# Kernel tuning notes

Measured on AMD Instinct MI355X. Metric: run time of the kernel, lower is better.

## Reference

```python
import jax, jax.numpy as jnp
import numpy as np

B, S, D, H, HD = 2, 4096, 768, 12, 64
W = 256           # one-sided window (attention_window=512)
C = S // W        # number of query chunks
NEG = -1e9


def _heads(x):
    # [B,S,D] -> [B,H,S,HD]
    return x.reshape(B, S, H, HD).transpose(0, 2, 1, 3)


def setup_inputs() -> dict:
    key = jax.random.key(0)
    ks = jax.random.split(key, 9)
    sc = 0.02
    w = lambda i: jax.random.normal(ks[i], (D, D), jnp.float32) * sc
    return {
        "hidden_states": jax.random.normal(ks[0], (B, S, D), jnp.float32),
        "Wq": w(1), "Wk": w(2), "Wv": w(3),
        "Wqg": w(4), "Wkg": w(5), "Wvg": w(6),
        "Wo": w(7),
        "attention_mask": jnp.ones((B, S), jnp.int32),
    }


def reference(hidden_states, Wq, Wk, Wv, Wqg, Wkg, Wvg, Wo, attention_mask):
    x = hidden_states
    scale = 1.0 / float(np.sqrt(HD))
    q = _heads(x @ Wq) * scale           # [B,H,S,HD]
    k = _heads(x @ Wk)
    v = _heads(x @ Wv)

    # ---- banded sliding-window attention (chunked, no [S,S] matrix) ----
    idx = jnp.arange(C)[:, None] * W + jnp.arange(3 * W)[None, :]   # [C,3W] into padded seq
    key_pos = idx - W                                               # absolute key position
    kp = jnp.pad(k, ((0, 0), (0, 0), (W, W), (0, 0)))
    vp = jnp.pad(v, ((0, 0), (0, 0), (W, W), (0, 0)))
    kc = kp[:, :, idx]                   # [B,H,C,3W,HD]
    vc = vp[:, :, idx]
    qc = q.reshape(B, H, C, W, HD)
    band = jnp.einsum('bhcqd,bhckd->bhcqk', qc, kc)  # [B,H,C,W,3W]

    qi = jnp.arange(W)[:, None]
    kj = jnp.arange(3 * W)[None, :]
    diag_ok = (kj >= qi) & (kj <= qi + 2 * W)              # |i-j| <= W
    valid = (key_pos >= 0) & (key_pos < S) & (key_pos != 0)  # in-range, dedupe global key 0
    mask = diag_ok[None, :, :] & valid[:, None, :]          # [C,W,3W]
    band = jnp.where(mask[None, None], band, NEG)

    # padding mask on keys
    m = jnp.where(attention_mask > 0, 0.0, NEG).astype(jnp.float32)  # [B,S]
    mp = jnp.pad(m, ((0, 0), (W, W)), constant_values=NEG)
    band = band + mp[:, idx][:, None, :, None, :]
    band = band.reshape(B, H, S, 3 * W)

    # every local query also attends to the global (CLS, pos 0) key
    gsc = jnp.einsum('bhsd,bhgd->bhsg', q, k[:, :, 0:1])   # [B,H,S,1]
    gsc = gsc + m[:, 0][:, None, None, None]

    scores = jnp.concatenate([gsc, band], axis=-1)          # [B,H,S,1+3W]
    probs = jax.nn.softmax(scores, axis=-1)
    pg = probs[..., :1]                                     # global-key prob
    pb = probs[..., 1:].reshape(B, H, C, W, 3 * W)
    out = jnp.einsum('bhcqk,bhckd->bhcqd', pb, vc).reshape(B, H, S, HD)
    out = out + pg * v[:, :, 0:1]

    # ---- global query (CLS) full attention with dedicated projections ----
    qg = _heads(x @ Wqg)[:, :, 0:1] * scale                 # [B,H,1,HD]
    kg = _heads(x @ Wkg)
    vg = _heads(x @ Wvg)
    gs = jnp.einsum('bhgd,bhsd->bhgs', qg, kg) + m[:, None, None, :]
    og = jnp.einsum('bhgs,bhsd->bhgd', jax.nn.softmax(gs, axis=-1), vg)
    out = out.at[:, :, 0:1].set(og)

    out = out.transpose(0, 2, 1, 3).reshape(B, S, D) @ Wo
    return out
```

## Files before the change

kernel.cpp:

```cpp
#include <hip/hip_runtime.h>

#define S_LEN 4096
#define NH 12
#define HDIM 64
#define DMODEL 768
#define NEGF -1.0e9f
#define TOK0_SPLITS 16

typedef __attribute__((ext_vector_type(8))) short bf16x8;
typedef __attribute__((ext_vector_type(4))) float f32x4;

__device__ __forceinline__ short f2b(float f) {
  union { float f; unsigned u; } v; v.f = f;
  unsigned r = v.u + 0x7fffu + ((v.u >> 16) & 1u);
  return (short)(r >> 16);
}
__device__ __forceinline__ float b2f(short s) {
  union { unsigned u; float f; } v; v.u = ((unsigned)(unsigned short)s) << 16;
  return v.f;
}

__global__ __launch_bounds__(256) void k_pre(const float* __restrict__ x,
                                             const float* __restrict__ Wq,
                                             const float* __restrict__ Wk,
                                             const float* __restrict__ Wv,
                                             const float* __restrict__ Wkg,
                                             const float* __restrict__ Wvg,
                                             const float* __restrict__ Wo,
                                             const float* __restrict__ Wqg,
                                             const int* __restrict__ amask,
                                             short* __restrict__ xb,
                                             short* __restrict__ W5t,
                                             short* __restrict__ Wot,
                                             float* __restrict__ qg,
                                             float* __restrict__ mvb) {
  __shared__ float smem[1056];
  int bid = blockIdx.x, tid = threadIdx.x;
  if (bid < 6144) {
    int i = bid * 256 + tid;
    float4 v = ((const float4*)x)[i];
    ((short4*)xb)[i] = make_short4(f2b(v.x), f2b(v.y), f2b(v.z), f2b(v.w));
  } else if (bid < 9600) {
    int zb = bid - 6144;
    int z = zb / 576, rem = zb - z * 576;
    int by = rem / 24, bx = rem - by * 24;
    const float* src; float scale = 1.f; short* dst;
    switch (z) {
      case 0: src = Wq;  scale = 0.125f * 1.44269504f; dst = W5t; break;
      case 1: src = Wk;  dst = W5t + 589824; break;
      case 2: src = Wv;  dst = W5t + 2 * 589824; break;
      case 3: src = Wkg; dst = W5t + 3 * 589824; break;
      case 4: src = Wvg; dst = W5t + 4 * 589824; break;
      default: src = Wo; dst = Wot; break;
    }
    int tx = tid & 31, ty = tid >> 5;
    int kb = by * 32, nb = bx * 32;
    for (int i = 0; i < 4; i++) smem[(ty + 8 * i) * 33 + tx] = src[(kb + ty + 8 * i) * 768 + nb + tx];
    __syncthreads();
    for (int i = 0; i < 4; i++)
      dst[(nb + ty + 8 * i) * 768 + kb + tx] = f2b(smem[tx * 33 + ty + 8 * i] * scale);
  } else if (bid < 9632) {
    int zb = bid - 9600;
    int b = zb >> 4, s = (zb & 15) * 256 + tid;
    mvb[b * S_LEN + s] = (s != 0 && amask[b * S_LEN + s] > 0) ? 0.f : NEGF;
  } else {
    int zb = bid - 9632;
    int h = zb % 12, b = zb / 12;
    int out = tid & 63, slice = tid >> 6;
    float* xr = smem;
    float* ps = smem + 768;
    for (int i = tid; i < 768; i += 256) xr[i] = x[(long)b * S_LEN * 768 + i];
    __syncthreads();
    float a = 0.f;
    int n = h * 64 + out;
#pragma unroll 8
    for (int k = slice * 192; k < slice * 192 + 192; k++) a += xr[k] * Wqg[k * 768 + n];
    ps[slice * 64 + out] = a;
    __syncthreads();
    if (tid < 64)
      qg[b * 768 + h * 64 + tid] = (ps[tid] + ps[64 + tid] + ps[128 + tid] + ps[192 + tid]) * 0.125f;
  }
}

__global__ __launch_bounds__(256) void k_gemm(const short* __restrict__ A,
                                              const short* __restrict__ Bt, int K, int mode,
                                              short* __restrict__ qkv, float* __restrict__ outf) {
  __shared__ short Al[2][128 * 32];
  __shared__ short Bl[2][128 * 32];
  int bid = blockIdx.x;
  int xcd = bid & 7, ii = bid >> 3;
  int bm = xcd * 8 + (ii & 7), bn = ii >> 3;
  int tid = threadIdx.x;
  int bm0 = bm * 128, bn0 = bn * 128;
  int w = tid >> 6, lane = tid & 63, g = lane >> 4, r16 = lane & 15;
  int wr = (w >> 1) * 64, wc = (w & 1) * 64;
  f32x4 zero4 = {0.f, 0.f, 0.f, 0.f};
  f32x4 acc[4][4];
  for (int m = 0; m < 4; m++) for (int n = 0; n < 4; n++) acc[m][n] = zero4;
  int srow = w * 32 + (lane >> 2);
  int scol = (lane & 3) * 8;
#define G_STAGE(BUF, KT)                                                              \
  do {                                                                                \
    for (int i = 0; i < 2; i++) {                                                     \
      const short* ga = &A[(long)(bm0 + srow + i * 16) * K + (KT) + scol];            \
      const short* gb = &Bt[(long)(bn0 + srow + i * 16) * K + (KT) + scol];           \
      __builtin_amdgcn_global_load_lds(                                               \
          (const __attribute__((address_space(1))) void*)ga,                          \
          (__attribute__((address_space(3))) void*)&Al[BUF][(w * 32 + i * 16) * 32],  \
          16, 0, 0);                                                                  \
      __builtin_amdgcn_global_load_lds(                                               \
          (const __attribute__((address_space(1))) void*)gb,                          \
          (__attribute__((address_space(3))) void*)&Bl[BUF][(w * 32 + i * 16) * 32],  \
          16, 0, 0);                                                                  \
    }                                                                                 \
  } while (0)
  int nt = K >> 5;
  G_STAGE(0, 0);
  __syncthreads();
  int cur = 0;
  for (int t = 0; t < nt; t++) {
    if (t + 1 < nt) G_STAGE(cur ^ 1, (t + 1) * 32);
    bf16x8 af[4], bfv[4];
    for (int m = 0; m < 4; m++) af[m] = *(const bf16x8*)&Al[cur][(wr + m * 16 + r16) * 32 + g * 8];
    for (int n = 0; n < 4; n++) bfv[n] = *(const bf16x8*)&Bl[cur][(wc + n * 16 + r16) * 32 + g * 8];
    for (int m = 0; m < 4; m++)
      for (int n = 0; n < 4; n++)
        acc[m][n] = __builtin_amdgcn_mfma_f32_16x16x32_bf16(af[m], bfv[n], acc[m][n], 0, 0, 0);
    __syncthreads();
    cur ^= 1;
  }
#undef G_STAGE
  for (int m = 0; m < 4; m++)
    for (int n = 0; n < 4; n++)
      for (int reg = 0; reg < 4; reg++) {
        int row = bm0 + wr + m * 16 + g * 4 + reg;
        int col = bn0 + wc + n * 16 + r16;
        float val = acc[m][n][reg];
        if (mode == 0) {
          int proj = col / 768;
          int rem = col - proj * 768;
          int hh = rem >> 6, d = rem & 63;
          int bb = row >> 12, s = row & 4095;
          qkv[(long)proj * 6291456 + ((((long)bb * NH + hh) * S_LEN + s) << 6) + d] = f2b(val);
        } else {
          outf[(long)row * 768 + col] = val;
        }
      }
}

__global__ __launch_bounds__(256) void k_vt(const short* __restrict__ V, short* __restrict__ Vt) {
  __shared__ short buf[64][72];
  int st = blockIdx.x, bh = blockIdx.y;
  int tid = threadIdx.x;
  long base = (long)bh * S_LEN * HDIM;
  int s0 = st * 64;
  int r = tid >> 2, c = (tid & 3) * 16;
  *(int4*)&buf[r][c]     = *(const int4*)&V[base + (long)(s0 + r) * HDIM + c];
  *(int4*)&buf[r][c + 8] = *(const int4*)&V[base + (long)(s0 + r) * HDIM + c + 8];
  __syncthreads();
  int d = tid >> 2, sc = (tid & 3) * 16;
  short tmp[16];
#pragma unroll
  for (int j = 0; j < 16; j++) tmp[j] = buf[sc + j][d];
  long ob = base + (long)d * S_LEN + s0 + sc;
  *(int4*)&Vt[ob]     = *(const int4*)&tmp[0];
  *(int4*)&Vt[ob + 8] = *(const int4*)&tmp[8];
}

#define KVPAD 36
#define PSTRIDE 68

__device__ __forceinline__ void band_chunk(
    int ks0, int qrow0, int g, int r16,
    const bf16x8 (&qf)[2][2], const bf16x8 (&kf)[4][2], const bf16x8 (&vf)[4][2],
    const float (&mv)[4],
    float (&mstate)[2][4], float (&lstate)[2][4], f32x4 (&acc)[2][4],
    short* Plds) {
  int dlo = ks0 - qrow0;
  bool fullok = (dlo >= -224) && (dlo <= 192);
  for (int m = 0; m < 2; m++) {
    f32x4 s[4];
    f32x4 zero4 = {0.f, 0.f, 0.f, 0.f};
    for (int n = 0; n < 4; n++) {
      f32x4 z = __builtin_amdgcn_mfma_f32_16x16x32_bf16(qf[m][0], kf[n][0], zero4, 0, 0, 0);
      s[n] = __builtin_amdgcn_mfma_f32_16x16x32_bf16(qf[m][1], kf[n][1], z, 0, 0, 0);
    }
    float p[4][4], rmax[4];
    for (int reg = 0; reg < 4; reg++) rmax[reg] = NEGF;
    if (fullok) {
      for (int n = 0; n < 4; n++)
        for (int reg = 0; reg < 4; reg++) {
          float val = s[n][reg] + mv[n];
          p[n][reg] = val;
          rmax[reg] = fmaxf(rmax[reg], val);
        }
    } else {
      int qbase = qrow0 + m * 16 + g * 4;
      for (int n = 0; n < 4; n++) {
        int kpos = ks0 + n * 16 + r16;
        for (int reg = 0; reg < 4; reg++) {
          int qpos = qbase + reg;
          bool ok = (kpos >= qpos - 256) && (kpos <= qpos + 256);
          float val = ok ? (s[n][reg] + mv[n]) : NEGF;
          p[n][reg] = val;
          rmax[reg] = fmaxf(rmax[reg], val);
        }
      }
    }
    for (int reg = 0; reg < 4; reg++) {
      float r = rmax[reg];
      r = fmaxf(r, __shfl_xor(r, 1));
      r = fmaxf(r, __shfl_xor(r, 2));
      r = fmaxf(r, __shfl_xor(r, 4));
      r = fmaxf(r, __shfl_xor(r, 8));
      rmax[reg] = r;
    }
    bool over = false;
    for (int reg = 0; reg < 4; reg++) over = over || (rmax[reg] > mstate[m][reg] + 8.f);
    if (__any((int)over)) {
      float scal[4];
      for (int reg = 0; reg < 4; reg++) {
        float mn = fmaxf(mstate[m][reg], rmax[reg]);
        scal[reg] = __builtin_amdgcn_exp2f(mstate[m][reg] - mn);
        mstate[m][reg] = mn;
      }
      float rs[4] = {0.f, 0.f, 0.f, 0.f};
      for (int n = 0; n < 4; n++)
        for (int reg = 0; reg < 4; reg++) {
          float e = __builtin_amdgcn_exp2f(p[n][reg] - mstate[m][reg]);
          p[n][reg] = e;
          rs[reg] += e;
        }
      for (int reg = 0; reg < 4; reg++) {
        float r = rs[reg];
        r += __shfl_xor(r, 1);
        r += __shfl_xor(r, 2);
        r += __shfl_xor(r, 4);
        r += __shfl_xor(r, 8);
        lstate[m][reg] = lstate[m][reg] * scal[reg] + r;
      }
      for (int n = 0; n < 4; n++)
        for (int reg = 0; reg < 4; reg++) acc[m][n][reg] *= scal[reg];
    } else {
      float rs[4] = {0.f, 0.f, 0.f, 0.f};
      for (int n = 0; n < 4; n++)
        for (int reg = 0; reg < 4; reg++) {
          float e = __builtin_amdgcn_exp2f(p[n][reg] - mstate[m][reg]);
          p[n][reg] = e;
          rs[reg] += e;
        }
      for (int reg = 0; reg < 4; reg++) {
        float r = rs[reg];
        r += __shfl_xor(r, 1);
        r += __shfl_xor(r, 2);
        r += __shfl_xor(r, 4);
        r += __shfl_xor(r, 8);
        lstate[m][reg] += r;
      }
    }
    for (int n = 0; n < 4; n++)
      for (int reg = 0; reg < 4; reg++)
        Plds[(g * 4 + reg) * PSTRIDE + n * 16 + r16] = f2b(p[n][reg]);
    bf16x8 pa[2];
    for (int ks = 0; ks < 2; ks++)
      pa[ks] = *(const bf16x8*)&Plds[r16 * PSTRIDE + ks * 32 + g * 8];
    for (int n = 0; n < 4; n++)
      for (int ks = 0; ks < 2; ks++)
        acc[m][n] = __builtin_amdgcn_mfma_f32_16x16x32_bf16(pa[ks], vf[n][ks], acc[m][n], 0, 0, 0);
  }
}

__global__ __launch_bounds__(256, 2) void k_band(const short* __restrict__ Qb,
                                                 const short* __restrict__ Kb,
                                                 const short* __restrict__ Vb,
                                                 const short* __restrict__ Vtb,
                                                 const int* __restrict__ amask,
                                                 const float* __restrict__ mvb,
                                                 short* __restrict__ oattn) {
  int qtb = blockIdx.x, h = blockIdx.y, b = blockIdx.z;
  int tid = threadIdx.x, w = tid >> 6, lane = tid & 63, g = lane >> 4, r16 = lane & 15;
  long bhof = ((long)(b * NH + h)) * S_LEN * HDIM;
  __shared__ short Klds[2][2][64][KVPAD];
  __shared__ short Vlds[2][2][64][KVPAD];
  __shared__ short Plds[4][16 * PSTRIDE];
  int qb0 = qtb * 128;
  int qrow0 = qb0 + w * 32;

  bf16x8 qf[2][2];
  for (int m = 0; m < 2; m++)
    for (int ks = 0; ks < 2; ks++)
      qf[m][ks] = *(const bf16x8*)&Qb[bhof + (long)(qrow0 + m * 16 + r16) * HDIM + ks * 32 + g * 8];

  float mstate[2][4], lstate[2][4];
  f32x4 acc[2][4];
  {
    bf16x8 k0f[2];
    for (int ks = 0; ks < 2; ks++) k0f[ks] = *(const bf16x8*)&Kb[bhof + ks * 32 + g * 8];
    float part[2];
    for (int m = 0; m < 2; m++) {
      float p = 0.f;
      for (int ks = 0; ks < 2; ks++)
        for (int j = 0; j < 8; j++) p += b2f(qf[m][ks][j]) * b2f(k0f[ks][j]);
      p += __shfl_xor(p, 16);
      p += __shfl_xor(p, 32);
      part[m] = p;
    }
    float mask0 = (amask[b * S_LEN] > 0) ? 0.f : NEGF;
    float v0v[4];
    for (int n = 0; n < 4; n++) v0v[n] = b2f(Vb[bhof + n * 16 + r16]);
    for (int m = 0; m < 2; m++)
      for (int reg = 0; reg < 4; reg++) {
        mstate[m][reg] = __shfl(part[m], g * 4 + reg) + mask0;
        lstate[m][reg] = 1.f;
        for (int n = 0; n < 4; n++) acc[m][n][reg] = v0v[n];
      }
  }

  int c0 = (qb0 - 256) >> 6; if (c0 < 0) c0 = 0;
  int c1 = (qb0 + 127 + 256) >> 6; if (c1 > 63) c1 = 63;
  int wlo = (qrow0 - 256) >> 6;
  int whi = (qrow0 + 31 + 256) >> 6;

  int ss = tid >> 2, qq = tid & 3;
  int ksh = qq >> 1, qcol = (qq & 1) * 16;
  int4 rk0, rk1, rv0, rv1;
#define STAGE_LOAD(CI)                                                              \
  do {                                                                              \
    int _k = (CI) * 64;                                                             \
    const int4* gk = (const int4*)&Kb[bhof + (long)(_k + ss) * HDIM + qq * 16];     \
    rk0 = gk[0]; rk1 = gk[1];                                                       \
    const int4* gv = (const int4*)&Vtb[bhof + (long)ss * S_LEN + _k + qq * 16];     \
    rv0 = gv[0]; rv1 = gv[1];                                                       \
  } while (0)
#define STAGE_WRITE(BUF)                                                            \
  do {                                                                              \
    short* kd = &Klds[BUF][ksh][ss][qcol];                                          \
    *(int4*)kd = rk0; *(int4*)(kd + 8) = rk1;                                       \
    short* vd = &Vlds[BUF][ksh][ss][qcol];                                          \
    *(int4*)vd = rv0; *(int4*)(vd + 8) = rv1;                                       \
  } while (0)

  STAGE_LOAD(c0);
  STAGE_WRITE(0);
  __syncthreads();

  for (int ci = c0; ci <= c1; ci++) {
    int buf = (ci - c0) & 1;
    bool havenext = (ci + 1 <= c1);
    if (havenext) STAGE_LOAD(ci + 1);
    if (ci >= wlo && ci <= whi) {
      int ks0 = ci * 64;
      bf16x8 kf[4][2], vf[4][2];
      for (int n = 0; n < 4; n++)
        for (int ks = 0; ks < 2; ks++) {
          kf[n][ks] = *(const bf16x8*)&Klds[buf][ks][n * 16 + r16][g * 8];
          vf[n][ks] = *(const bf16x8*)&Vlds[buf][ks][n * 16 + r16][g * 8];
        }
      float mv[4];
      for (int n = 0; n < 4; n++) mv[n] = mvb[b * S_LEN + ks0 + n * 16 + r16];
      band_chunk(ks0, qrow0, g, r16, qf, kf, vf, mv, mstate, lstate, acc, &Plds[w][0]);
    }
    if (havenext) STAGE_WRITE(buf ^ 1);
    __syncthreads();
  }
#undef STAGE_LOAD
#undef STAGE_WRITE

  for (int m = 0; m < 2; m++)
    for (int n = 0; n < 4; n++)
      for (int reg = 0; reg < 4; reg++) {
        int token = qrow0 + m * 16 + g * 4 + reg;
        int col = h * 64 + n * 16 + r16;
        oattn[((long)b * S_LEN + token) * 768 + col] = f2b(acc[m][n][reg] / lstate[m][reg]);
      }
}

__global__ __launch_bounds__(256) void k_tok0_part(const float* __restrict__ qg,
                                                   const short* __restrict__ Kg,
                                                   const short* __restrict__ Vg,
                                                   const int* __restrict__ amask,
                                                   float* __restrict__ part) {
  int split = blockIdx.x, bhid = blockIdx.y;
  int b = bhid / NH, h = bhid % NH;
  long base = (long)bhid * S_LEN * HDIM;
  int tid = threadIdx.x, lane = tid & 63, w = tid >> 6;
  int s = split * 256 + tid;
  __shared__ float qgl[64];
  __shared__ float p_sh[256];
  __shared__ float red[4];
  __shared__ float psum[4][64];
  if (tid < 64) qgl[tid] = qg[b * 768 + h * 64 + tid];
  __syncthreads();
  float dot = 0.f;
  {
    const int4* kr = (const int4*)&Kg[base + (long)s * HDIM];
#pragma unroll
    for (int u = 0; u < 8; u++) {
      int4 pk = kr[u];
      const short* sp = (const short*)&pk;
      for (int j = 0; j < 8; j++) dot += qgl[u * 8 + j] * b2f(sp[j]);
    }
    dot += (amask[b * S_LEN + s] > 0) ? 0.f : NEGF;
  }
  float mx = dot;
  for (int o = 32; o; o >>= 1) mx = fmaxf(mx, __shfl_xor(mx, o));
  if (lane == 0) red[w] = mx;
  __syncthreads();
  mx = fmaxf(fmaxf(red[0], red[1]), fmaxf(red[2], red[3]));
  float e = __expf(dot - mx);
  p_sh[tid] = e;
  float sum = e;
  for (int o = 32; o; o >>= 1) sum += __shfl_xor(sum, o);
  __syncthreads();
  if (lane == 0) red[w] = sum;
  __syncthreads();
  sum = red[0] + red[1] + red[2] + red[3];
  int d = tid & 63, grp = tid >> 6;
  float a = 0.f;
  long vb = base + (long)(split * 256 + grp * 64) * HDIM + d;
#pragma unroll 8
  for (int j = 0; j < 64; j++) a += p_sh[grp * 64 + j] * b2f(Vg[vb + (long)j * HDIM]);
  psum[grp][d] = a;
  __syncthreads();
  float* dst = &part[((long)bhid * TOK0_SPLITS + split) * 66];
  if (tid == 0) { dst[0] = mx; dst[1] = sum; }
  if (tid < 64) dst[2 + tid] = psum[0][tid] + psum[1][tid] + psum[2][tid] + psum[3][tid];
}

__global__ void k_tok0_comb(const float* __restrict__ part, short* __restrict__ oattn) {
  int bhid = blockIdx.x, d = threadIdx.x;
  int b = bhid / NH, h = bhid % NH;
  const float* p0 = &part[(long)bhid * TOK0_SPLITS * 66];
  float M = NEGF;
  for (int i = 0; i < TOK0_SPLITS; i++) M = fmaxf(M, p0[i * 66]);
  float L = 0.f, a = 0.f;
  for (int i = 0; i < TOK0_SPLITS; i++) {
    float sc = __expf(p0[i * 66] - M);
    L += sc * p0[i * 66 + 1];
    a += sc * p0[i * 66 + 2 + d];
  }
  oattn[((long)b * S_LEN) * 768 + h * 64 + d] = f2b(a / L);
}

extern "C" void kernel_launch(void* const* d_in, const int* in_sizes, int n_in,
                              void* d_out, int out_size, void* d_ws, size_t ws_size,
                              hipStream_t stream) {
  (void)in_sizes; (void)n_in; (void)out_size; (void)ws_size;
  const float* x   = (const float*)d_in[0];
  const float* Wq  = (const float*)d_in[1];
  const float* Wk  = (const float*)d_in[2];
  const float* Wv  = (const float*)d_in[3];
  const float* Wqg = (const float*)d_in[4];
  const float* Wkg = (const float*)d_in[5];
  const float* Wvg = (const float*)d_in[6];
  const float* Wo  = (const float*)d_in[7];
  const int* amask = (const int*)d_in[8];
  char* ws = (char*)d_ws;
  short* xb    = (short*)(ws);
  short* Vt    = (short*)(ws);
  short* W5t   = (short*)(ws + 12582912);
  short* Wot   = (short*)(ws + 18481152);
  short* qkv   = (short*)(ws + 19660800);
  short* oattn = (short*)(ws + 82575360);
  float* qgbuf = (float*)(ws + 95158272);
  float* partb = (float*)(ws + 95164416);
  float* mvb   = (float*)(ws + 95265792);
  float* outf  = (float*)d_out;

  k_pre<<<9656, 256, 0, stream>>>(x, Wq, Wk, Wv, Wkg, Wvg, Wo, Wqg, amask,
                                  xb, W5t, Wot, qgbuf, mvb);
  k_gemm<<<1920, 256, 0, stream>>>(xb, W5t, 768, 0, qkv, nullptr);
  const short* Qb = qkv;
  const short* Kb = qkv + 6291456;
  const short* Vb = qkv + 2 * 6291456;
  const short* Kg = qkv + 3 * 6291456;
  const short* Vg = qkv + 4 * 6291456;
  k_vt<<<dim3(64, 24), 256, 0, stream>>>(Vb, Vt);
  k_band<<<dim3(32, 12, 2), 256, 0, stream>>>(Qb, Kb, Vb, Vt, amask, mvb, oattn);
  k_tok0_part<<<dim3(TOK0_SPLITS, 24), 256, 0, stream>>>(qgbuf, Kg, Vg, amask, partb);
  k_tok0_comb<<<24, 64, 0, stream>>>(partb, oattn);
  k_gemm<<<384, 256, 0, stream>>>(oattn, Wot, 768, 1, nullptr, outf);
}
```

Baseline: 215.2 us.

## Merge band attention and global-token partial kernels into one launch

```diff
diff --git a/kernel.cpp b/kernel.cpp
--- a/kernel.cpp
+++ b/kernel.cpp
@@ -270,161 +270,163 @@
   }
 }
 
-__global__ __launch_bounds__(256, 2) void k_band(const short* __restrict__ Qb,
+__global__ __launch_bounds__(256, 4) void k_attn(const short* __restrict__ Qb,
                                                  const short* __restrict__ Kb,
                                                  const short* __restrict__ Vb,
                                                  const short* __restrict__ Vtb,
+                                                 const short* __restrict__ Kg,
+                                                 const short* __restrict__ Vg,
+                                                 const float* __restrict__ qg,
                                                  const int* __restrict__ amask,
                                                  const float* __restrict__ mvb,
-                                                 short* __restrict__ oattn) {
-  int qtb = blockIdx.x, h = blockIdx.y, b = blockIdx.z;
-  int tid = threadIdx.x, w = tid >> 6, lane = tid & 63, g = lane >> 4, r16 = lane & 15;
-  long bhof = ((long)(b * NH + h)) * S_LEN * HDIM;
+                                                 short* __restrict__ oattn,
+                                                 float* __restrict__ part) {
   __shared__ short Klds[2][2][64][KVPAD];
-  __shared__ short Vlds[2][2][64][KVPAD];
   __shared__ short Plds[4][16 * PSTRIDE];
-  int qb0 = qtb * 128;
-  int qrow0 = qb0 + w * 32;
-
-  bf16x8 qf[2][2];
-  for (int m = 0; m < 2; m++)
-    for (int ks = 0; ks < 2; ks++)
-      qf[m][ks] = *(const bf16x8*)&Qb[bhof + (long)(qrow0 + m * 16 + r16) * HDIM + ks * 32 + g * 8];
-
-  float mstate[2][4], lstate[2][4];
-  f32x4 acc[2][4];
-  {
-    bf16x8 k0f[2];
-    for (int ks = 0; ks < 2; ks++) k0f[ks] = *(const bf16x8*)&Kb[bhof + ks * 32 + g * 8];
-    float part[2];
-    for (int m = 0; m < 2; m++) {
-      float p = 0.f;
+  __shared__ float fsm[592];
+  int bid = blockIdx.x, tid = threadIdx.x;
+  if (bid < 768) {
+    int qtb = bid & 31, rest = bid >> 5;
+    int h = rest % NH, b = rest / NH;
+    int w = tid >> 6, lane = tid & 63, g = lane >> 4, r16 = lane & 15;
+    long bhof = ((long)(b * NH + h)) * S_LEN * HDIM;
+    int qb0 = qtb * 128;
+    int qrow0 = qb0 + w * 32;
+
+    bf16x8 qf[2][2];
+    for (int m = 0; m < 2; m++)
       for (int ks = 0; ks < 2; ks++)
-        for (int j = 0; j < 8; j++) p += b2f(qf[m][ks][j]) * b2f(k0f[ks][j]);
-      p += __shfl_xor(p, 16);
-      p += __shfl_xor(p, 32);
-      part[m] = p;
-    }
-    float mask0 = (amask[b * S_LEN] > 0) ? 0.f : NEGF;
-    float v0v[4];
-    for (int n = 0; n < 4; n++) v0v[n] = b2f(Vb[bhof + n * 16 + r16]);
-    for (int m = 0; m < 2; m++)
-      for (int reg = 0; reg < 4; reg++) {
-        mstate[m][reg] = __shfl(part[m], g * 4 + reg) + mask0;
-        lstate[m][reg] = 1.f;
-        for (int n = 0; n < 4; n++) acc[m][n][reg] = v0v[n];
-      }
-  }
-
-  int c0 = (qb0 - 256) >> 6; if (c0 < 0) c0 = 0;
-  int c1 = (qb0 + 127 + 256) >> 6; if (c1 > 63) c1 = 63;
-  int wlo = (qrow0 - 256) >> 6;
-  int whi = (qrow0 + 31 + 256) >> 6;
-
-  int ss = tid >> 2, qq = tid & 3;
-  int ksh = qq >> 1, qcol = (qq & 1) * 16;
-  int4 rk0, rk1, rv0, rv1;
+        qf[m][ks] = *(const bf16x8*)&Qb[bhof + (long)(qrow0 + m * 16 + r16) * HDIM + ks * 32 + g * 8];
+
+    float mstate[2][4], lstate[2][4];
+    f32x4 acc[2][4];
+    {
+      bf16x8 k0f[2];
+      for (int ks = 0; ks < 2; ks++) k0f[ks] = *(const bf16x8*)&Kb[bhof + ks * 32 + g * 8];
+      float part0[2];
+      for (int m = 0; m < 2; m++) {
+        float p = 0.f;
+        for (int ks = 0; ks < 2; ks++)
+          for (int j = 0; j < 8; j++) p += b2f(qf[m][ks][j]) * b2f(k0f[ks][j]);
+        p += __shfl_xor(p, 16);
+        p += __shfl_xor(p, 32);
+        part0[m] = p;
+      }
+      float mask0 = (amask[b * S_LEN] > 0) ? 0.f : NEGF;
+      float v0v[4];
+      for (int n = 0; n < 4; n++) v0v[n] = b2f(Vb[bhof + n * 16 + r16]);
+      for (int m = 0; m < 2; m++)
+        for (int reg = 0; reg < 4; reg++) {
+          mstate[m][reg] = __shfl(part0[m], g * 4 + reg) + mask0;
+          lstate[m][reg] = 1.f;
+          for (int n = 0; n < 4; n++) acc[m][n][reg] = v0v[n];
+        }
+    }
+
+    int c0 = (qb0 - 256) >> 6; if (c0 < 0) c0 = 0;
+    int c1 = (qb0 + 127 + 256) >> 6; if (c1 > 63) c1 = 63;
+    int wlo = (qrow0 - 256) >> 6;
+    int whi = (qrow0 + 31 + 256) >> 6;
+
+    int ss = tid >> 2, qq = tid & 3;
+    int ksh = qq >> 1, qcol = (qq & 1) * 16;
+    int4 rk0, rk1;
 #define STAGE_LOAD(CI)                                                              \
-  do {                                                                              \
-    int _k = (CI) * 64;                                                             \
-    const int4* gk = (const int4*)&Kb[bhof + (long)(_k + ss) * HDIM + qq * 16];     \
-    rk0 = gk[0]; rk1 = gk[1];                                                       \
-    const int4* gv = (const int4*)&Vtb[bhof + (long)ss * S_LEN + _k + qq * 16];     \
-    rv0 = gv[0]; rv1 = gv[1];                                                       \
-  } while (0)
+    do {                                                                            \
+      int _k = (CI) * 64;                                                           \
+      const int4* gk = (const int4*)&Kb[bhof + (long)(_k + ss) * HDIM + qq * 16];   \
+      rk0 = gk[0]; rk1 = gk[1];                                                     \
+    } while (0)
 #define STAGE_WRITE(BUF)                                                            \
-  do {                                                                              \
-    short* kd = &Klds[BUF][ksh][ss][qcol];                                          \
-    *(int4*)kd = rk0; *(int4*)(kd + 8) = rk1;                                       \
-    short* vd = &Vlds[BUF][ksh][ss][qcol];                                          \
-    *(int4*)vd = rv0; *(int4*)(vd + 8) = rv1;                                       \
-  } while (0)
-
-  STAGE_LOAD(c0);
-  STAGE_WRITE(0);
-  __syncthreads();
-
-  for (int ci = c0; ci <= c1; ci++) {
-    int buf = (ci - c0) & 1;
-    bool havenext = (ci + 1 <= c1);
-    if (havenext) STAGE_LOAD(ci + 1);
-    if (ci >= wlo && ci <= whi) {
-      int ks0 = ci * 64;
-      bf16x8 kf[4][2], vf[4][2];
-      for (int n = 0; n < 4; n++)
-        for (int ks = 0; ks < 2; ks++) {
-          kf[n][ks] = *(const bf16x8*)&Klds[buf][ks][n * 16 + r16][g * 8];
-          vf[n][ks] = *(const bf16x8*)&Vlds[buf][ks][n * 16 + r16][g * 8];
-        }
-      float mv[4];
-      for (int n = 0; n < 4; n++) mv[n] = mvb[b * S_LEN + ks0 + n * 16 + r16];
-      band_chunk(ks0, qrow0, g, r16, qf, kf, vf, mv, mstate, lstate, acc, &Plds[w][0]);
-    }
-    if (havenext) STAGE_WRITE(buf ^ 1);
-    __syncthreads();
-  }
+    do {                                                                            \
+      short* kd = &Klds[BUF][ksh][ss][qcol];                                        \
+      *(int4*)kd = rk0; *(int4*)(kd + 8) = rk1;                                     \
+    } while (0)
+
+    STAGE_LOAD(c0);
+    STAGE_WRITE(0);
+    __syncthreads();
+
+    for (int ci = c0; ci <= c1; ci++) {
+      int buf = (ci - c0) & 1;
+      bool havenext = (ci + 1 <= c1);
+      if (havenext) STAGE_LOAD(ci + 1);
+      if (ci >= wlo && ci <= whi) {
+        int ks0 = ci * 64;
+        bf16x8 vf[4][2];
+        for (int n = 0; n < 4; n++)
+          for (int ks = 0; ks < 2; ks++)
+            vf[n][ks] = *(const bf16x8*)&Vtb[bhof + (long)(n * 16 + r16) * S_LEN + ks0 + ks * 32 + g * 8];
+        float mv[4];
+        for (int n = 0; n < 4; n++) mv[n] = mvb[b * S_LEN + ks0 + n * 16 + r16];
+        bf16x8 kf[4][2];
+        for (int n = 0; n < 4; n++)
+          for (int ks = 0; ks < 2; ks++)
+            kf[n][ks] = *(const bf16x8*)&Klds[buf][ks][n * 16 + r16][g * 8];
+        band_chunk(ks0, qrow0, g, r16, qf, kf, vf, mv, mstate, lstate, acc, &Plds[w][0]);
+      }
+      if (havenext) STAGE_WRITE(buf ^ 1);
+      __syncthreads();
+    }
 #undef STAGE_LOAD
 #undef STAGE_WRITE
 
-  for (int m = 0; m < 2; m++)
-    for (int n = 0; n < 4; n++)
-      for (int reg = 0; reg < 4; reg++) {
-        int token = qrow0 + m * 16 + g * 4 + reg;
-        int col = h * 64 + n * 16 + r16;
-        oattn[((long)b * S_LEN + token) * 768 + col] = f2b(acc[m][n][reg] / lstate[m][reg]);
-      }
-}
-
-__global__ __launch_bounds__(256) void k_tok0_part(const float* __restrict__ qg,
-                                                   const short* __restrict__ Kg,
-                                                   const short* __restrict__ Vg,
-                                                   const int* __restrict__ amask,
-                                                   float* __restrict__ part) {
-  int split = blockIdx.x, bhid = blockIdx.y;
-  int b = bhid / NH, h = bhid % NH;
-  long base = (long)bhid * S_LEN * HDIM;
-  int tid = threadIdx.x, lane = tid & 63, w = tid >> 6;
-  int s = split * 256 + tid;
-  __shared__ float qgl[64];
-  __shared__ float p_sh[256];
-  __shared__ float red[4];
-  __shared__ float psum[4][64];
-  if (tid < 64) qgl[tid] = qg[b * 768 + h * 64 + tid];
-  __syncthreads();
-  float dot = 0.f;
-  {
-    const int4* kr = (const int4*)&Kg[base + (long)s * HDIM];
+    for (int m = 0; m < 2; m++)
+      for (int n = 0; n < 4; n++)
+        for (int reg = 0; reg < 4; reg++) {
+          int token = qrow0 + m * 16 + g * 4 + reg;
+          int col = h * 64 + n * 16 + r16;
+          oattn[((long)b * S_LEN + token) * 768 + col] = f2b(acc[m][n][reg] / lstate[m][reg]);
+        }
+  } else {
+    int tbid = bid - 768;
+    int split = tbid & 15, bhid = tbid >> 4;
+    int b = bhid / NH, h = bhid % NH;
+    long base = (long)bhid * S_LEN * HDIM;
+    int lane = tid & 63, w = tid >> 6;
+    int s = split * 256 + tid;
+    float* qgl  = fsm;
+    float* p_sh = fsm + 64;
+    float* red  = fsm + 320;
+    float* psum = fsm + 324;
+    if (tid < 64) qgl[tid] = qg[b * 768 + h * 64 + tid];
+    __syncthreads();
+    float dot = 0.f;
+    {
+      const int4* kr = (const int4*)&Kg[base + (long)s * HDIM];
 #pragma unroll
-    for (int u = 0; u < 8; u++) {
-      int4 pk = kr[u];
-      const short* sp = (const short*)&pk;
-      for (int j = 0; j < 8; j++) dot += qgl[u * 8 + j] * b2f(sp[j]);
-    }
-    dot += (amask[b * S_LEN + s] > 0) ? 0.f : NEGF;
+      for (int u = 0; u < 8; u++) {
+        int4 pk = kr[u];
+        const short* sp = (const short*)&pk;
+        for (int j = 0; j < 8; j++) dot += qgl[u * 8 + j] * b2f(sp[j]);
+      }
+      dot += (amask[b * S_LEN + s] > 0) ? 0.f : NEGF;
+    }
+    float mx = dot;
+    for (int o = 32; o; o >>= 1) mx = fmaxf(mx, __shfl_xor(mx, o));
+    if (lane == 0) red[w] = mx;
+    __syncthreads();
+    mx = fmaxf(fmaxf(red[0], red[1]), fmaxf(red[2], red[3]));
+    float e = __expf(dot - mx);
+    p_sh[tid] = e;
+    float sum = e;
+    for (int o = 32; o; o >>= 1) sum += __shfl_xor(sum, o);
+    __syncthreads();
+    if (lane == 0) red[w] = sum;
+    __syncthreads();
+    sum = red[0] + red[1] + red[2] + red[3];
+    int d = tid & 63, grp = tid >> 6;
+    float a = 0.f;
+    long vb = base + (long)(split * 256 + grp * 64) * HDIM + d;
+#pragma unroll 8
+    for (int j = 0; j < 64; j++) a += p_sh[grp * 64 + j] * b2f(Vg[vb + (long)j * HDIM]);
+    psum[grp * 64 + d] = a;
+    __syncthreads();
+    float* dst = &part[((long)bhid * TOK0_SPLITS + split) * 66];
+    if (tid == 0) { dst[0] = mx; dst[1] = sum; }
+    if (tid < 64)
+      dst[2 + tid] = psum[tid] + psum[64 + tid] + psum[128 + tid] + psum[192 + tid];
   }
-  float mx = dot;
-  for (int o = 32; o; o >>= 1) mx = fmaxf(mx, __shfl_xor(mx, o));
-  if (lane == 0) red[w] = mx;
-  __syncthreads();
-  mx = fmaxf(fmaxf(red[0], red[1]), fmaxf(red[2], red[3]));
-  float e = __expf(dot - mx);
-  p_sh[tid] = e;
-  float sum = e;
-  for (int o = 32; o; o >>= 1) sum += __shfl_xor(sum, o);
-  __syncthreads();
-  if (lane == 0) red[w] = sum;
-  __syncthreads();
-  sum = red[0] + red[1] + red[2] + red[3];
-  int d = tid & 63, grp = tid >> 6;
-  float a = 0.f;
-  long vb = base + (long)(split * 256 + grp * 64) * HDIM + d;
-#pragma unroll 8
-  for (int j = 0; j < 64; j++) a += p_sh[grp * 64 + j] * b2f(Vg[vb + (long)j * HDIM]);
-  psum[grp][d] = a;
-  __syncthreads();
-  float* dst = &part[((long)bhid * TOK0_SPLITS + split) * 66];
-  if (tid == 0) { dst[0] = mx; dst[1] = sum; }
-  if (tid < 64) dst[2 + tid] = psum[0][tid] + psum[1][tid] + psum[2][tid] + psum[3][tid];
 }
 
 __global__ void k_tok0_comb(const float* __restrict__ part, short* __restrict__ oattn) {
@@ -476,8 +478,7 @@
   const short* Kg = qkv + 3 * 6291456;
   const short* Vg = qkv + 4 * 6291456;
   k_vt<<<dim3(64, 24), 256, 0, stream>>>(Vb, Vt);
-  k_band<<<dim3(32, 12, 2), 256, 0, stream>>>(Qb, Kb, Vb, Vt, amask, mvb, oattn);
-  k_tok0_part<<<dim3(TOK0_SPLITS, 24), 256, 0, stream>>>(qgbuf, Kg, Vg, amask, partb);
+  k_attn<<<1152, 256, 0, stream>>>(Qb, Kb, Vb, Vt, Kg, Vg, qgbuf, amask, mvb, oattn, partb);
   k_tok0_comb<<<24, 64, 0, stream>>>(partb, oattn);
   k_gemm<<<384, 256, 0, stream>>>(oattn, Wot, 768, 1, nullptr, outf);
 }
```

Result: slower. 386.4 us (+79.5%).
